# Optimization experiments

Hardware: AMD Instinct MI355X
Metric: run time of the kernel (lower is better)

Reference implementation:

```python
import jax, jax.numpy as jnp
import numpy as np

HEAD_SIZE = 64


def setup_inputs() -> dict:
    key = jax.random.key(0)
    ks = jax.random.split(key, 10)
    B, S, D, H, hs = 4, 2048, 768, 12, HEAD_SIZE
    F = 4 * D
    sd = lambda n: 1.0 / np.sqrt(n)
    return {
        "x": jax.random.normal(ks[0], (B, S, D), jnp.float32),
        "Wq": jax.random.normal(ks[1], (H, D, hs), jnp.float32) * sd(D),
        "Wk": jax.random.normal(ks[2], (H, D, hs), jnp.float32) * sd(D),
        "Wv": jax.random.normal(ks[3], (H, D, hs), jnp.float32) * sd(D),
        "Wo": jax.random.normal(ks[4], (D, D), jnp.float32) * sd(D),
        "bo": jnp.zeros((D,), jnp.float32),
        "W1": jax.random.normal(ks[5], (D, F), jnp.float32) * sd(D),
        "b1": jnp.zeros((F,), jnp.float32),
        "W2": jax.random.normal(ks[6], (F, D), jnp.float32) * sd(F),
        "b2": jnp.zeros((D,), jnp.float32),
    }


def reference(x, Wq, Wk, Wv, Wo, bo, W1, b1, W2, b2):
    B, S, D = x.shape
    hs = Wq.shape[-1]
    # per-head projections (no bias), vectorized over heads: [B,H,S,hs]
    q = jnp.einsum("bsd,hde->bhse", x, Wq)
    k = jnp.einsum("bsd,hde->bhse", x, Wk)
    v = jnp.einsum("bsd,hde->bhse", x, Wv)
    # causal attention scores [B,H,S,S], scaled by sqrt(head_size)
    scores = jnp.einsum("bhse,bhte->bhst", q, k) / jnp.sqrt(jnp.float32(hs))
    causal = jnp.tril(jnp.ones((S, S), dtype=bool))
    scores = jnp.where(causal, scores, -jnp.inf)
    attn = jax.nn.softmax(scores, axis=-1)
    z = jnp.einsum("bhst,bhte->bhse", attn, v)
    # concat heads along feature dim (head order preserved) -> [B,S,D]
    z = z.transpose(0, 2, 1, 3).reshape(B, S, D)
    # output projection + residual
    z = z @ Wo + bo + x
    # FFN + residual
    h = jax.nn.relu(z @ W1 + b1)
    return h @ W2 + b2 + z
```

## Files before the change

kernel.cpp:

```cpp
#include <hip/hip_runtime.h>


typedef __attribute__((ext_vector_type(4))) float f32x4;
typedef __attribute__((ext_vector_type(8))) short bf16x8;
typedef __attribute__((ext_vector_type(4))) unsigned short u16x4;

#define GLB_AS __attribute__((address_space(1)))
#define LDS_AS __attribute__((address_space(3)))

__device__ __forceinline__ unsigned short f2bf(float f) {
  unsigned int u = __float_as_uint(f);
  u = (u + 0x7FFFu + ((u >> 16) & 1u)) >> 16;
  return (unsigned short)u;
}

__device__ __forceinline__ void gload16(const void* g, void* l) {
  __builtin_amdgcn_global_load_lds((const GLB_AS unsigned int*)g,
                                   (LDS_AS unsigned int*)l, 16, 0, 0);
}

__device__ __forceinline__ int xcd_swz(int orig, int nwg) {
  int q = nwg >> 3, r = nwg & 7;
  int xcd = orig & 7, rest = orig >> 3;
  return (xcd < r ? xcd * (q + 1) : r * (q + 1) + (xcd - r) * q) + rest;
}

#define VMW4 asm volatile("s_waitcnt vmcnt(4)" ::: "memory")
#define VMW3 asm volatile("s_waitcnt vmcnt(3)" ::: "memory")
#define VMW0 asm volatile("s_waitcnt vmcnt(0)" ::: "memory")

__global__ void prep(const float* __restrict__ x, unsigned short* __restrict__ xb,
                     const float* __restrict__ Wq, const float* __restrict__ Wk,
                     const float* __restrict__ Wv, unsigned short* __restrict__ wqkvT,
                     const float* __restrict__ Wo, const float* __restrict__ W1,
                     const float* __restrict__ W2, unsigned short* __restrict__ woT,
                     unsigned short* __restrict__ w1T, unsigned short* __restrict__ w2T,
                     float qscale) {
  __shared__ float tile[32][33];
  const int id = blockIdx.x;
  const int tid = threadIdx.x;

  if (id < 6144) {
    int i = (id * 256 + tid) * 4;
    float4 f = *(const float4*)&x[i];
    u16x4 o;
    o[0] = f2bf(f.x); o[1] = f2bf(f.y); o[2] = f2bf(f.z); o[3] = f2bf(f.w);
    *(u16x4*)&xb[i] = o;
    return;
  }

  const int tx = tid & 31, ty = tid >> 5;
  const float* in; unsigned short* out; int C, R, bx, by; float scale = 1.0f;

  if (id < 7872) {
    int id2 = id - 6144;
    int z = id2 / 48, rem = id2 % 48;
    int wsel = z / 12, head = z % 12;
    R = 768; C = 64;
    in = (wsel == 0 ? Wq : wsel == 1 ? Wk : Wv) + (size_t)head * R * C;
    out = wqkvT + (size_t)wsel * R * R + (size_t)head * R * C;
    if (wsel == 0) scale = qscale;
    bx = (rem & 1) * 32; by = (rem >> 1) * 32;
  } else {
    int id3 = id - 7872;
    int gx;
    if (id3 < 576)       {             in = Wo; out = woT; C = 768;  gx = 24; R = 768; }
    else if (id3 < 2880) { id3 -= 576;  in = W1; out = w1T; C = 3072; gx = 96; R = 768; }
    else                 { id3 -= 2880; in = W2; out = w2T; C = 768;  gx = 24; R = 3072; }
    bx = (id3 % gx) * 32; by = (id3 / gx) * 32;
  }

  #pragma unroll
  for (int i = 0; i < 32; i += 8)
    tile[ty + i][tx] = in[(size_t)(by + ty + i) * C + bx + tx];
  __syncthreads();
  #pragma unroll
  for (int i = 0; i < 32; i += 8)
    out[(size_t)(bx + ty + i) * R + by + tx] = f2bf(tile[tx][ty + i] * scale);
}

__global__ void vtrans(const unsigned short* __restrict__ v, unsigned short* __restrict__ vT) {
  __shared__ unsigned short tile[32][33];
  int bh = blockIdx.z, b = bh / 12, h = bh % 12;
  int s0 = blockIdx.x * 32, e0 = blockIdx.y * 32;
  int tx = threadIdx.x, ty = threadIdx.y;
  #pragma unroll
  for (int i = 0; i < 32; i += 8)
    tile[ty + i][tx] = v[(size_t)(b * 2048 + s0 + ty + i) * 768 + h * 64 + e0 + tx];
  __syncthreads();
  #pragma unroll
  for (int i = 0; i < 32; i += 8)
    vT[(size_t)((b * 12 + h) * 64 + e0 + ty + i) * 2048 + s0 + tx] = tile[tx][ty + i];
}

template <int EPI>
__global__ void gemm_bf16(const unsigned short* __restrict__ A,
                          const unsigned short* __restrict__ Bt,
                          const float* __restrict__ bias,
                          const float* __restrict__ resid,
                          float* __restrict__ Cf,
                          unsigned short* __restrict__ Cb,
                          int M, int N, int K, int gy) {
  __shared__ unsigned short Alds[2][128 * 32];
  __shared__ unsigned short Blds[2][128 * 32];
  const int tid = threadIdx.x;
  const int lane = tid & 63;
  const int w = tid >> 6;
  const int wm = w & 1, wn = w >> 1;
  const int wg = xcd_swz(blockIdx.x, gridDim.x);
  const int gsz = 8 * gy;
  const int group = wg / gsz;
  const int rem = wg - group * gsz;
  const int bm = (group * 8 + (rem & 7)) * 128;
  const int bn = (rem >> 3) * 128;

  f32x4 acc[4][4] = {};

  const int r0 = tid >> 2;
  const int c0 = (tid & 3) * 8;

  #pragma unroll
  for (int i = 0; i < 2; ++i) {
    int row = r0 + i * 64;
    gload16(&A[(size_t)(bm + row) * K + c0], &Alds[0][row * 32 + c0]);
    gload16(&Bt[(size_t)(bn + row) * K + c0], &Blds[0][row * 32 + c0]);
  }
  __syncthreads();

  int buf = 0;
  for (int k0 = 0; k0 < K; k0 += 32) {
    if (k0 + 32 < K) {
      #pragma unroll
      for (int i = 0; i < 2; ++i) {
        int row = r0 + i * 64;
        gload16(&A[(size_t)(bm + row) * K + k0 + 32 + c0], &Alds[buf ^ 1][row * 32 + c0]);
        gload16(&Bt[(size_t)(bn + row) * K + k0 + 32 + c0], &Blds[buf ^ 1][row * 32 + c0]);
      }
      VMW4;
    } else {
      VMW0;
    }
    __builtin_amdgcn_s_barrier();

    bf16x8 af[4], bf[4];
    #pragma unroll
    for (int m = 0; m < 4; ++m)
      af[m] = *(const bf16x8*)&Alds[buf][(wm * 64 + m * 16 + (lane & 15)) * 32 + (lane >> 4) * 8];
    #pragma unroll
    for (int n = 0; n < 4; ++n)
      bf[n] = *(const bf16x8*)&Blds[buf][(wn * 64 + n * 16 + (lane & 15)) * 32 + (lane >> 4) * 8];
    #pragma unroll
    for (int m = 0; m < 4; ++m)
      #pragma unroll
      for (int n = 0; n < 4; ++n)
        acc[m][n] = __builtin_amdgcn_mfma_f32_16x16x32_bf16(af[m], bf[n], acc[m][n], 0, 0, 0);

    __builtin_amdgcn_s_barrier();
    buf ^= 1;
  }

  const int crow0 = bm + wm * 64 + ((lane >> 4)) * 4;
  const int ccol0 = bn + wn * 64 + (lane & 15);
  #pragma unroll
  for (int m = 0; m < 4; ++m) {
    #pragma unroll
    for (int n = 0; n < 4; ++n) {
      int col = ccol0 + n * 16;
      #pragma unroll
      for (int r = 0; r < 4; ++r) {
        int row = crow0 + m * 16 + r;
        float v = acc[m][n][r];
        if constexpr (EPI & 1) v += bias[col];
        if constexpr (EPI & 4) v += resid[(size_t)row * N + col];
        if constexpr (EPI & 2) v = fmaxf(v, 0.f);
        if constexpr (EPI & 8) Cf[(size_t)row * N + col] = v;
        if constexpr (EPI & 16) Cb[(size_t)row * N + col] = f2bf(v);
      }
    }
  }
}

#define BSTG(bb, kt) {                                                     \
    _Pragma("unroll") for (int i = 0; i < 2; ++i) {                        \
      int ch = tid + 512 * i;                                              \
      gload16(&A[(size_t)(bm + (ch >> 2)) * K + (kt) + (ch & 3) * 8],      \
              &Alds[bb][(ch >> 2) * 32 + (ch & 3) * 8]);                   \
    }                                                                      \
    gload16(&Bt[(size_t)(bn + (tid >> 2)) * K + (kt) + (tid & 3) * 8],     \
            &Blds[bb][(tid >> 2) * 32 + (tid & 3) * 8]); }

template <int EPI>
__global__ __launch_bounds__(512, 2)
void gemm_big(const unsigned short* __restrict__ A,
              const unsigned short* __restrict__ Bt,
              const float* __restrict__ bias,
              unsigned short* __restrict__ Cb,
              int M, int N, int K, int gy, size_t segN) {
  __shared__ unsigned short Alds[2][256 * 32];
  __shared__ unsigned short Blds[2][128 * 32];
  const int tid = threadIdx.x;
  const int lane = tid & 63;
  const int w = tid >> 6;
  const int wr = w >> 1, wc = w & 1;
  const int q16 = lane & 15, qt = lane >> 4;

  const int wg = xcd_swz(blockIdx.x, gridDim.x);
  const int gsz = 8 * gy;
  const int group = wg / gsz;
  const int rem = wg - group * gsz;
  const int bm = (group * 8 + (rem & 7)) * 256;
  const int bn = (rem >> 3) * 128;

  f32x4 acc[4][4] = {};

  BSTG(0, 0);
  __syncthreads();

  int buf = 0;
  for (int k0 = 0; k0 < K; k0 += 32) {
    if (k0 + 32 < K) {
      BSTG(buf ^ 1, k0 + 32);
      VMW3;
    } else {
      VMW0;
    }
    __builtin_amdgcn_s_barrier();

    bf16x8 af[4], bf[4];
    #pragma unroll
    for (int m = 0; m < 4; ++m)
      af[m] = *(const bf16x8*)&Alds[buf][(wr * 64 + m * 16 + q16) * 32 + qt * 8];
    #pragma unroll
    for (int n = 0; n < 4; ++n)
      bf[n] = *(const bf16x8*)&Blds[buf][(wc * 64 + n * 16 + q16) * 32 + qt * 8];
    #pragma unroll
    for (int m = 0; m < 4; ++m)
      #pragma unroll
      for (int n = 0; n < 4; ++n)
        acc[m][n] = __builtin_amdgcn_mfma_f32_16x16x32_bf16(af[m], bf[n], acc[m][n], 0, 0, 0);

    __builtin_amdgcn_s_barrier();
    buf ^= 1;
  }

  const int crow0 = bm + wr * 64 + qt * 4;
  const int ccol0 = bn + wc * 64 + q16;
  const int seg = bn / 768;
  const int lcol0 = (bn % 768) + wc * 64 + q16;
  #pragma unroll
  for (int m = 0; m < 4; ++m) {
    #pragma unroll
    for (int n = 0; n < 4; ++n) {
      int col = ccol0 + n * 16;
      #pragma unroll
      for (int r = 0; r < 4; ++r) {
        int row = crow0 + m * 16 + r;
        float v = acc[m][n][r];
        if constexpr (EPI & 1) v += bias[col];
        if constexpr (EPI & 2) v = fmaxf(v, 0.f);
        if constexpr (EPI & 16) Cb[(size_t)row * N + col] = f2bf(v);
        if constexpr (EPI & 32)
          Cb[(size_t)seg * segN + (size_t)row * 768 + lcol0 + n * 16] = f2bf(v);
      }
    }
  }
}

__global__ void attn_fwd(const unsigned short* __restrict__ q,
                         const unsigned short* __restrict__ k,
                         const unsigned short* __restrict__ vT,
                         unsigned short* __restrict__ z) {
  __shared__ unsigned short Klds[2 * 2 * 64 * 32];
  __shared__ unsigned short Vlds[2 * 2 * 64 * 32];
  __shared__ unsigned short Plds[4 * 16 * 72];

  const int wgid = xcd_swz(blockIdx.x, gridDim.x);
  const int pi = wgid & 15;
  const int bh = wgid >> 4;
  const int b = bh / 12, h = bh % 12;
  const int tid = threadIdx.x, lane = tid & 63, w = tid >> 6;
  const int q16 = lane & 15;
  const int qt  = lane >> 4;
  const int rdc = ((qt ^ ((q16 >> 1) & 3)) * 8);

  const int srow = tid >> 2;
  const int sdc  = (tid & 3) * 8;
  const int sgc  = (((tid & 3) ^ ((srow >> 1) & 3)) * 8);
  const size_t kbase = (size_t)(b * 2048) * 768 + h * 64;
  const size_t vbase = (size_t)((b * 12 + h) * 64) * 2048;
  unsigned short* Pw = &Plds[w * 16 * 72];

  #pragma unroll 1
  for (int seg = 0; seg < 2; ++seg) {
    const int qb = seg == 0 ? pi : 31 - pi;
    const int q0 = qb * 64;
    const int nt = qb + 1;

    const int qrow = q0 + w * 16 + q16;
    const size_t qoff = (size_t)(b * 2048 + qrow) * 768 + h * 64 + qt * 8;
    bf16x8 qf0 = *(const bf16x8*)&q[qoff];
    bf16x8 qf1 = *(const bf16x8*)&q[qoff + 32];

    f32x4 accO[4] = {};
    float lrow = 0.f;

    #pragma unroll
    for (int i = 0; i < 2; ++i) {
      gload16(&k[kbase + (size_t)srow * 768 + i * 32 + sgc],
              &Klds[i * 2048 + srow * 32 + sdc]);
      gload16(&vT[vbase + (size_t)srow * 2048 + i * 32 + sgc],
              &Vlds[i * 2048 + srow * 32 + sdc]);
    }
    __syncthreads();

    int buf = 0;
    for (int t = 0; t < nt; ++t) {
      if (t + 1 < nt) {
        const int kv1 = (t + 1) * 64;
        const int bo = (buf ^ 1) * 4096;
        #pragma unroll
        for (int i = 0; i < 2; ++i) {
          gload16(&k[kbase + (size_t)(kv1 + srow) * 768 + i * 32 + sgc],
                  &Klds[bo + i * 2048 + srow * 32 + sdc]);
          gload16(&vT[vbase + (size_t)srow * 2048 + kv1 + i * 32 + sgc],
                  &Vlds[bo + i * 2048 + srow * 32 + sdc]);
        }
        VMW4;
      } else {
        VMW0;
      }
      __builtin_amdgcn_s_barrier();

      const int kv0 = t * 64;
      const int kb_ = buf * 4096;

      bf16x8 kf0[4], kf1[4];
      #pragma unroll
      for (int n = 0; n < 4; ++n) {
        kf0[n] = *(const bf16x8*)&Klds[kb_ + 0 * 2048 + (n * 16 + q16) * 32 + rdc];
        kf1[n] = *(const bf16x8*)&Klds[kb_ + 1 * 2048 + (n * 16 + q16) * 32 + rdc];
      }
      f32x4 s[4];
      __builtin_amdgcn_s_setprio(1);
      #pragma unroll
      for (int n = 0; n < 4; ++n) {
        f32x4 zz = {};
        s[n] = __builtin_amdgcn_mfma_f32_16x16x32_bf16(kf0[n], qf0, zz, 0, 0, 0);
      }
      #pragma unroll
      for (int n = 0; n < 4; ++n)
        s[n] = __builtin_amdgcn_mfma_f32_16x16x32_bf16(kf1[n], qf1, s[n], 0, 0, 0);
      __builtin_amdgcn_s_setprio(0);

      if (t == nt - 1) {
        const int rowg = q0 + w * 16 + q16;
        #pragma unroll
        for (int n = 0; n < 4; ++n)
          #pragma unroll
          for (int r = 0; r < 4; ++r)
            if (kv0 + n * 16 + qt * 4 + r > rowg) s[n][r] = -3.0e38f;
      }

      #pragma unroll
      for (int n = 0; n < 4; ++n)
        #pragma unroll
        for (int r = 0; r < 4; ++r) { s[n][r] = exp2f(s[n][r]); lrow += s[n][r]; }

      #pragma unroll
      for (int n = 0; n < 4; ++n) {
        unsigned int lo, hi;
        asm("v_cvt_pk_bf16_f32 %0, %1, %2" : "=v"(lo) : "v"(s[n][0]), "v"(s[n][1]));
        asm("v_cvt_pk_bf16_f32 %0, %1, %2" : "=v"(hi) : "v"(s[n][2]), "v"(s[n][3]));
        uint2 pk; pk.x = lo; pk.y = hi;
        *(uint2*)&Pw[q16 * 72 + n * 16 + qt * 4] = pk;
      }

      __builtin_amdgcn_s_setprio(1);
      #pragma unroll
      for (int kk = 0; kk < 2; ++kk) {
        bf16x8 pf = *(const bf16x8*)&Pw[q16 * 72 + kk * 32 + qt * 8];
        #pragma unroll
        for (int n = 0; n < 4; ++n) {
          bf16x8 vf = *(const bf16x8*)&Vlds[kb_ + kk * 2048 + (n * 16 + q16) * 32 + rdc];
          accO[n] = __builtin_amdgcn_mfma_f32_16x16x32_bf16(pf, vf, accO[n], 0, 0, 0);
        }
      }
      __builtin_amdgcn_s_setprio(0);

      __builtin_amdgcn_s_barrier();
      buf ^= 1;
    }

    lrow += __shfl_xor(lrow, 16);
    lrow += __shfl_xor(lrow, 32);
    #pragma unroll
    for (int r = 0; r < 4; ++r) {
      float lr = __int_as_float(__builtin_amdgcn_ds_bpermute((qt * 4 + r) * 4,
                                                             __float_as_int(lrow)));
      float linv = 1.0f / lr;
      int rowg = q0 + w * 16 + qt * 4 + r;
      #pragma unroll
      for (int n = 0; n < 4; ++n)
        z[(size_t)(b * 2048 + rowg) * 768 + h * 64 + n * 16 + q16]
            = f2bf(accO[n][r] * linv);
    }
  }
}

extern "C" void kernel_launch(void* const* d_in, const int* in_sizes, int n_in,
                              void* d_out, int out_size, void* d_ws, size_t ws_size,
                              hipStream_t stream) {
  const float* x  = (const float*)d_in[0];
  const float* Wq = (const float*)d_in[1];
  const float* Wk = (const float*)d_in[2];
  const float* Wv = (const float*)d_in[3];
  const float* Wo = (const float*)d_in[4];
  const float* bo = (const float*)d_in[5];
  const float* W1 = (const float*)d_in[6];
  const float* b1 = (const float*)d_in[7];
  const float* W2 = (const float*)d_in[8];
  const float* b2 = (const float*)d_in[9];
  float* out = (float*)d_out;

  const int B = 4, S = 2048, D = 768, H = 12, hs = 64, F = 3072;
  const int M = B * S;
  const size_t MD = (size_t)M * D;

  unsigned short* xb   = (unsigned short*)d_ws;
  unsigned short* qb   = xb + MD;
  unsigned short* kb   = qb + MD;
  unsigned short* vb   = kb + MD;
  unsigned short* hbuf = xb;
  unsigned short* vT   = vb + MD;
  unsigned short* zb   = vT + MD;
  float*          z2f  = (float*)(zb + MD);
  unsigned short* z2b  = (unsigned short*)(z2f + MD);
  unsigned short* wqkvT= z2b + MD;
  unsigned short* woT  = wqkvT + 3 * (size_t)D * D;
  unsigned short* w1T  = woT + (size_t)D * D;
  unsigned short* w2T  = w1T + (size_t)D * F;

  const float QS = 0.125f * 1.4426950408889634f;

  prep<<<dim3(13056), 256, 0, stream>>>(x, xb, Wq, Wk, Wv, wqkvT,
                                        Wo, W1, W2, woT, w1T, w2T, QS);

  {
    int gy = 3 * D / 128;
    gemm_big<32><<<dim3(32 * gy), 512, 0, stream>>>(xb, wqkvT, nullptr, qb,
                                                    M, 3 * D, D, gy, MD);
  }

  vtrans<<<dim3(S / 32, hs / 32, B * H), dim3(32, 8), 0, stream>>>(vb, vT);

  attn_fwd<<<dim3((S / 128) * B * H), 256, 0, stream>>>(qb, kb, vT, zb);

  {
    int gy = D / 128;
    gemm_bf16<1 | 4 | 8 | 16><<<dim3(64 * gy), 256, 0, stream>>>(zb, woT, bo, x,
                                                                 z2f, z2b, M, D, D, gy);
  }
  {
    int gy = F / 128;
    gemm_big<1 | 2 | 16><<<dim3(32 * gy), 512, 0, stream>>>(z2b, w1T, b1, hbuf,
                                                            M, F, D, gy, 0);
  }
  {
    int gy = D / 128;
    gemm_bf16<1 | 4 | 8><<<dim3(64 * gy), 256, 0, stream>>>(hbuf, w2T, b2, z2f,
                                                            out, nullptr, M, D, F, gy);
  }
}
```

Baseline: 268.9 us.

## Split K across two wave groups in FFN down-projection GEMM

Adds a 512-thread GEMM kernel for the F->D projection in which two groups of four waves each process half of the K dimension with their own double-buffered LDS tiles. The partial accumulators are then reduced through shared memory before the bias and residual epilogue. The aim is more waves per output tile and more latency hiding for this long-K, narrow-N GEMM, at the cost of an LDS reduction step and higher LDS use per block.

Result: faster. 263.4 us (-2.0%).

```diff
diff --git a/kernel.cpp b/kernel.cpp
--- a/kernel.cpp
+++ b/kernel.cpp
@@ -180,6 +180,120 @@
   }
 }
 
+template <int EPI>
+__global__ __launch_bounds__(512, 2)
+void gemm_skb(const unsigned short* __restrict__ A,
+              const unsigned short* __restrict__ Bt,
+              const float* __restrict__ bias,
+              const float* __restrict__ resid,
+              float* __restrict__ Cf,
+              int M, int N, int K, int gy) {
+  __shared__ unsigned short SH[32768];
+  const int tid = threadIdx.x;
+  const int lane = tid & 63;
+  const int w = tid >> 6;
+  const int pk = w >> 2;
+  const int wl = w & 3;
+  const int wm = wl & 1, wn = wl >> 1;
+
+  const int wg = xcd_swz(blockIdx.x, gridDim.x);
+  const int gsz = 8 * gy;
+  const int group = wg / gsz;
+  const int rem = wg - group * gsz;
+  const int bm = (group * 8 + (rem & 7)) * 128;
+  const int bn = (rem >> 3) * 128;
+
+  const int Kh = K >> 1;
+  const int kof = pk * Kh;
+  unsigned short* Abase = SH + pk * 8192;
+  unsigned short* Bbase = SH + 16384 + pk * 8192;
+
+  f32x4 acc[4][4] = {};
+
+  const int st = tid & 255;
+  const int r0 = st >> 2;
+  const int c0 = (st & 3) * 8;
+
+  #pragma unroll
+  for (int i = 0; i < 2; ++i) {
+    int row = r0 + i * 64;
+    gload16(&A[(size_t)(bm + row) * K + kof + c0], &Abase[row * 32 + c0]);
+    gload16(&Bt[(size_t)(bn + row) * K + kof + c0], &Bbase[row * 32 + c0]);
+  }
+  __syncthreads();
+
+  int buf = 0;
+  for (int k0 = 0; k0 < Kh; k0 += 32) {
+    if (k0 + 32 < Kh) {
+      #pragma unroll
+      for (int i = 0; i < 2; ++i) {
+        int row = r0 + i * 64;
+        gload16(&A[(size_t)(bm + row) * K + kof + k0 + 32 + c0],
+                &Abase[(buf ^ 1) * 4096 + row * 32 + c0]);
+        gload16(&Bt[(size_t)(bn + row) * K + kof + k0 + 32 + c0],
+                &Bbase[(buf ^ 1) * 4096 + row * 32 + c0]);
+      }
+      VMW4;
+    } else {
+      VMW0;
+    }
+    __builtin_amdgcn_s_barrier();
+
+    bf16x8 af[4], bf[4];
+    #pragma unroll
+    for (int m = 0; m < 4; ++m)
+      af[m] = *(const bf16x8*)&Abase[buf * 4096 + (wm * 64 + m * 16 + (lane & 15)) * 32 + (lane >> 4) * 8];
+    #pragma unroll
+    for (int n = 0; n < 4; ++n)
+      bf[n] = *(const bf16x8*)&Bbase[buf * 4096 + (wn * 64 + n * 16 + (lane & 15)) * 32 + (lane >> 4) * 8];
+    #pragma unroll
+    for (int m = 0; m < 4; ++m)
+      #pragma unroll
+      for (int n = 0; n < 4; ++n)
+        acc[m][n] = __builtin_amdgcn_mfma_f32_16x16x32_bf16(af[m], bf[n], acc[m][n], 0, 0, 0);
+
+    __builtin_amdgcn_s_barrier();
+    buf ^= 1;
+  }
+
+  __syncthreads();
+  float* ex = (float*)SH;
+  if (pk == 1) {
+    #pragma unroll
+    for (int m = 0; m < 4; ++m)
+      #pragma unroll
+      for (int n = 0; n < 4; ++n)
+        *(f32x4*)&ex[((m * 4 + n) * 1024 + st * 4)] = acc[m][n];
+  }
+  __syncthreads();
+  if (pk == 0) {
+    #pragma unroll
+    for (int m = 0; m < 4; ++m)
+      #pragma unroll
+      for (int n = 0; n < 4; ++n) {
+        f32x4 o = *(const f32x4*)&ex[((m * 4 + n) * 1024 + st * 4)];
+        acc[m][n] += o;
+      }
+    const int crow0 = bm + wm * 64 + (lane >> 4) * 4;
+    const int ccol0 = bn + wn * 64 + (lane & 15);
+    #pragma unroll
+    for (int m = 0; m < 4; ++m) {
+      #pragma unroll
+      for (int n = 0; n < 4; ++n) {
+        int col = ccol0 + n * 16;
+        #pragma unroll
+        for (int r = 0; r < 4; ++r) {
+          int row = crow0 + m * 16 + r;
+          float v = acc[m][n][r];
+          if constexpr (EPI & 1) v += bias[col];
+          if constexpr (EPI & 4) v += resid[(size_t)row * N + col];
+          Cf[(size_t)row * N + col] = v;
+        }
+      }
+    }
+  }
+}
+
 #define BSTG(bb, kt) {                                                     \
     _Pragma("unroll") for (int i = 0; i < 2; ++i) {                        \
       int ch = tid + 512 * i;                                              \
@@ -467,7 +581,7 @@
   }
   {
     int gy = D / 128;
-    gemm_bf16<1 | 4 | 8><<<dim3(64 * gy), 256, 0, stream>>>(hbuf, w2T, b2, z2f,
-                                                            out, nullptr, M, D, F, gy);
-  }
-}
+    gemm_skb<1 | 4><<<dim3(64 * gy), 512, 0, stream>>>(hbuf, w2T, b2, z2f,
+                                                       out, M, D, F, gy);
+  }
+}
```

## Split K across two wave groups in narrow GEMMs with LDS reduction

Applied to the files above, without the earlier changes.

Replaces the 256-thread output-projection and FFN-down GEMMs with a 512-thread split-K kernel. Two groups of four waves each process half of K in separate LDS buffers, then sum their partial accumulators through LDS before the epilogue. This is meant to put more waves on each CU for these narrow (N=768) GEMMs, which launch only 384 blocks, and to shorten each block's serial K loop. In exchange it uses twice the LDS per block and adds a cross-group reduction with extra barriers.

Result: faster. 262.8 us (-2.3%).

```diff
diff --git a/kernel.cpp b/kernel.cpp
--- a/kernel.cpp
+++ b/kernel.cpp
@@ -94,19 +94,22 @@
 }
 
 template <int EPI>
-__global__ void gemm_bf16(const unsigned short* __restrict__ A,
-                          const unsigned short* __restrict__ Bt,
-                          const float* __restrict__ bias,
-                          const float* __restrict__ resid,
-                          float* __restrict__ Cf,
-                          unsigned short* __restrict__ Cb,
-                          int M, int N, int K, int gy) {
-  __shared__ unsigned short Alds[2][128 * 32];
-  __shared__ unsigned short Blds[2][128 * 32];
+__global__ __launch_bounds__(512, 2)
+void gemm_skb(const unsigned short* __restrict__ A,
+              const unsigned short* __restrict__ Bt,
+              const float* __restrict__ bias,
+              const float* __restrict__ resid,
+              float* __restrict__ Cf,
+              unsigned short* __restrict__ Cb,
+              int M, int N, int K, int gy) {
+  __shared__ unsigned short SH[32768];
   const int tid = threadIdx.x;
   const int lane = tid & 63;
   const int w = tid >> 6;
-  const int wm = w & 1, wn = w >> 1;
+  const int pk = w >> 2;
+  const int wl = w & 3;
+  const int wm = wl & 1, wn = wl >> 1;
+
   const int wg = xcd_swz(blockIdx.x, gridDim.x);
   const int gsz = 8 * gy;
   const int group = wg / gsz;
@@ -114,27 +117,35 @@
   const int bm = (group * 8 + (rem & 7)) * 128;
   const int bn = (rem >> 3) * 128;
 
+  const int Kh = K >> 1;
+  const int kof = pk * Kh;
+  unsigned short* Abase = SH + pk * 8192;
+  unsigned short* Bbase = SH + 16384 + pk * 8192;
+
   f32x4 acc[4][4] = {};
 
-  const int r0 = tid >> 2;
-  const int c0 = (tid & 3) * 8;
+  const int st = tid & 255;
+  const int r0 = st >> 2;
+  const int c0 = (st & 3) * 8;
 
   #pragma unroll
   for (int i = 0; i < 2; ++i) {
     int row = r0 + i * 64;
-    gload16(&A[(size_t)(bm + row) * K + c0], &Alds[0][row * 32 + c0]);
-    gload16(&Bt[(size_t)(bn + row) * K + c0], &Blds[0][row * 32 + c0]);
+    gload16(&A[(size_t)(bm + row) * K + kof + c0], &Abase[row * 32 + c0]);
+    gload16(&Bt[(size_t)(bn + row) * K + kof + c0], &Bbase[row * 32 + c0]);
   }
   __syncthreads();
 
   int buf = 0;
-  for (int k0 = 0; k0 < K; k0 += 32) {
-    if (k0 + 32 < K) {
+  for (int k0 = 0; k0 < Kh; k0 += 32) {
+    if (k0 + 32 < Kh) {
       #pragma unroll
       for (int i = 0; i < 2; ++i) {
         int row = r0 + i * 64;
-        gload16(&A[(size_t)(bm + row) * K + k0 + 32 + c0], &Alds[buf ^ 1][row * 32 + c0]);
-        gload16(&Bt[(size_t)(bn + row) * K + k0 + 32 + c0], &Blds[buf ^ 1][row * 32 + c0]);
+        gload16(&A[(size_t)(bm + row) * K + kof + k0 + 32 + c0],
+                &Abase[(buf ^ 1) * 4096 + row * 32 + c0]);
+        gload16(&Bt[(size_t)(bn + row) * K + kof + k0 + 32 + c0],
+                &Bbase[(buf ^ 1) * 4096 + row * 32 + c0]);
       }
       VMW4;
     } else {
@@ -145,10 +156,10 @@
     bf16x8 af[4], bf[4];
     #pragma unroll
     for (int m = 0; m < 4; ++m)
-      af[m] = *(const bf16x8*)&Alds[buf][(wm * 64 + m * 16 + (lane & 15)) * 32 + (lane >> 4) * 8];
+      af[m] = *(const bf16x8*)&Abase[buf * 4096 + (wm * 64 + m * 16 + (lane & 15)) * 32 + (lane >> 4) * 8];
     #pragma unroll
     for (int n = 0; n < 4; ++n)
-      bf[n] = *(const bf16x8*)&Blds[buf][(wn * 64 + n * 16 + (lane & 15)) * 32 + (lane >> 4) * 8];
+      bf[n] = *(const bf16x8*)&Bbase[buf * 4096 + (wn * 64 + n * 16 + (lane & 15)) * 32 + (lane >> 4) * 8];
     #pragma unroll
     for (int m = 0; m < 4; ++m)
       #pragma unroll
@@ -159,22 +170,40 @@
     buf ^= 1;
   }
 
-  const int crow0 = bm + wm * 64 + ((lane >> 4)) * 4;
-  const int ccol0 = bn + wn * 64 + (lane & 15);
-  #pragma unroll
-  for (int m = 0; m < 4; ++m) {
-    #pragma unroll
-    for (int n = 0; n < 4; ++n) {
-      int col = ccol0 + n * 16;
-      #pragma unroll
-      for (int r = 0; r < 4; ++r) {
-        int row = crow0 + m * 16 + r;
-        float v = acc[m][n][r];
-        if constexpr (EPI & 1) v += bias[col];
-        if constexpr (EPI & 4) v += resid[(size_t)row * N + col];
-        if constexpr (EPI & 2) v = fmaxf(v, 0.f);
-        if constexpr (EPI & 8) Cf[(size_t)row * N + col] = v;
-        if constexpr (EPI & 16) Cb[(size_t)row * N + col] = f2bf(v);
+  __syncthreads();
+  float* ex = (float*)SH;
+  if (pk == 1) {
+    #pragma unroll
+    for (int m = 0; m < 4; ++m)
+      #pragma unroll
+      for (int n = 0; n < 4; ++n)
+        *(f32x4*)&ex[((m * 4 + n) * 1024 + st * 4)] = acc[m][n];
+  }
+  __syncthreads();
+  if (pk == 0) {
+    #pragma unroll
+    for (int m = 0; m < 4; ++m)
+      #pragma unroll
+      for (int n = 0; n < 4; ++n) {
+        f32x4 o = *(const f32x4*)&ex[((m * 4 + n) * 1024 + st * 4)];
+        acc[m][n] += o;
+      }
+    const int crow0 = bm + wm * 64 + (lane >> 4) * 4;
+    const int ccol0 = bn + wn * 64 + (lane & 15);
+    #pragma unroll
+    for (int m = 0; m < 4; ++m) {
+      #pragma unroll
+      for (int n = 0; n < 4; ++n) {
+        int col = ccol0 + n * 16;
+        #pragma unroll
+        for (int r = 0; r < 4; ++r) {
+          int row = crow0 + m * 16 + r;
+          float v = acc[m][n][r];
+          if constexpr (EPI & 1) v += bias[col];
+          if constexpr (EPI & 4) v += resid[(size_t)row * N + col];
+          if constexpr (EPI & 8) Cf[(size_t)row * N + col] = v;
+          if constexpr (EPI & 16) Cb[(size_t)row * N + col] = f2bf(v);
+        }
       }
     }
   }
@@ -457,8 +486,8 @@
 
   {
     int gy = D / 128;
-    gemm_bf16<1 | 4 | 8 | 16><<<dim3(64 * gy), 256, 0, stream>>>(zb, woT, bo, x,
-                                                                 z2f, z2b, M, D, D, gy);
+    gemm_skb<1 | 4 | 8 | 16><<<dim3(64 * gy), 512, 0, stream>>>(
+        zb, woT, bo, x, z2f, z2b, M, D, D, gy);
   }
   {
     int gy = F / 128;
@@ -467,7 +496,7 @@
   }
   {
     int gy = D / 128;
-    gemm_bf16<1 | 4 | 8><<<dim3(64 * gy), 256, 0, stream>>>(hbuf, w2T, b2, z2f,
-                                                            out, nullptr, M, D, F, gy);
-  }
-}
+    gemm_skb<1 | 4 | 8><<<dim3(64 * gy), 512, 0, stream>>>(
+        hbuf, w2T, b2, z2f, out, nullptr, M, D, F, gy);
+  }
+}
```
